# Kernel optimization log

Hardware: AMD Instinct MI355X
Metric: run time of the kernel (lower is better)

The kernel has to match this reference:

```python
import jax, jax.numpy as jnp
import numpy as np


def setup_inputs() -> dict:
    key = jax.random.key(0)
    k1, k2, k3, k4 = jax.random.split(key, 4)
    B, T, S, D = 32, 512, 1024, 1024
    inp = jax.random.normal(k1, (B, T, D), dtype=jnp.float32)
    ctx = jax.random.normal(k2, (B, S, D), dtype=jnp.float32)
    W_in = jax.random.normal(k3, (D, D), dtype=jnp.float32) * (1.0 / np.sqrt(D))
    W_out = jax.random.normal(k4, (D, 2 * D), dtype=jnp.float32) * (1.0 / np.sqrt(2 * D))
    return {"input": inp, "context": ctx, "W_in": W_in, "W_out": W_out}


def reference(input, context, W_in, W_out):
    # GlobalAttention, attn_type='general', no mask, no coverage, tgt_len > 1.
    B, T, D = input.shape
    S = context.shape[1]
    # score: (W_in h_t) . h_s   -> [B, T, S]
    h_t = jnp.einsum('btd,ed->bte', input, W_in)           # linear_in (no bias)
    align = jnp.einsum('btd,bsd->bts', h_t, context)
    align_vectors = jax.nn.softmax(align, axis=-1)          # [B, T, S]
    # weighted sum of context
    c = jnp.einsum('bts,bsd->btd', align_vectors, context)  # [B, T, D]
    # concat [c, input] -> linear_out (no bias for 'general') -> tanh
    concat_c = jnp.concatenate([c, input], axis=-1)          # [B, T, 2D]
    attn_h = jnp.tanh(jnp.einsum('btf,df->btd', concat_c, W_out))
    # not one_step: transpose to [T, B, ...]
    attn_h = jnp.transpose(attn_h, (1, 0, 2))
    align_vectors = jnp.transpose(align_vectors, (1, 0, 2))
    return attn_h, align_vectors
```

## Files before the change

kernel.cpp:

```cpp
#include <hip/hip_runtime.h>
#include <hip/hip_bf16.h>


typedef short bf16x8 __attribute__((ext_vector_type(8)));
typedef float f32x4 __attribute__((ext_vector_type(4)));
typedef unsigned short us;

#define NB 32
#define NT_ 512
#define NS 1024
#define ND 1024

__device__ inline us f2bf(float x) {
  unsigned u = __float_as_uint(x);
  u += 0x7FFFu + ((u >> 16) & 1u);
  return (us)(u >> 16);
}
__device__ inline float bf2f(us h) { return __uint_as_float(((unsigned)h) << 16); }

__device__ inline void store_split(us* __restrict__ hi, us* __restrict__ lo, size_t idx, float v) {
  us h = f2bf(v);
  hi[idx] = h;
  lo[idx] = f2bf(v - bf2f(h));
}

__global__ void ga_split(const float* __restrict__ src, us* __restrict__ hi,
                         us* __restrict__ lo, long n) {
  long i0 = ((long)blockIdx.x * blockDim.x + threadIdx.x) * 4;
  long stride = (long)gridDim.x * blockDim.x * 4;
  for (long i = i0; i < n; i += stride) {
    float4 v = *reinterpret_cast<const float4*>(src + i);
    ushort4 h, l;
    h.x = f2bf(v.x); l.x = f2bf(v.x - bf2f(h.x));
    h.y = f2bf(v.y); l.y = f2bf(v.y - bf2f(h.y));
    h.z = f2bf(v.z); l.z = f2bf(v.z - bf2f(h.z));
    h.w = f2bf(v.w); l.w = f2bf(v.w - bf2f(h.w));
    *reinterpret_cast<ushort4*>(hi + i) = h;
    *reinterpret_cast<ushort4*>(lo + i) = l;
  }
}

__global__ void ga_cvt(const float* __restrict__ src, us* __restrict__ dst, long n) {
  long i0 = ((long)blockIdx.x * blockDim.x + threadIdx.x) * 4;
  long stride = (long)gridDim.x * blockDim.x * 4;
  for (long i = i0; i < n; i += stride) {
    float4 v = *reinterpret_cast<const float4*>(src + i);
    ushort4 h;
    h.x = f2bf(v.x); h.y = f2bf(v.y); h.z = f2bf(v.z); h.w = f2bf(v.w);
    *reinterpret_cast<ushort4*>(dst + i) = h;
  }
}

__global__ void ga_transpose_split(const float* __restrict__ ctx, us* __restrict__ tHi,
                                   us* __restrict__ tLo) {
  __shared__ float tile[64][65];
  int s0 = blockIdx.x << 6, d0 = blockIdx.y << 6, b = blockIdx.z;
  const float* src = ctx + (size_t)b * NS * ND;
  int tid = threadIdx.x;
#pragma unroll
  for (int i = 0; i < 16; ++i) {
    int lin = (i << 8) + tid;
    int r = lin >> 6, c = lin & 63;
    tile[r][c] = src[(size_t)(s0 + r) * ND + d0 + c];
  }
  __syncthreads();
  us* oH = tHi + (size_t)b * ND * NS;
  us* oL = tLo + (size_t)b * ND * NS;
#pragma unroll
  for (int i = 0; i < 16; ++i) {
    int lin = (i << 8) + tid;
    int dr = lin >> 6, sc = lin & 63;
    float v = tile[sc][dr];
    size_t o = (size_t)(d0 + dr) * NS + s0 + sc;
    us h = f2bf(v);
    oH[o] = h;
    oL[o] = f2bf(v - bf2f(h));
  }
}

__global__ __launch_bounds__(256) void ga_softmax(float* __restrict__ al,
                                                  us* __restrict__ pHi, us* __restrict__ pLo) {
  int row = blockIdx.x;
  int tid = threadIdx.x;
  float* p = al + (size_t)row * NS;
  float4 v = *reinterpret_cast<const float4*>(p + (tid << 2));
  float m = fmaxf(fmaxf(v.x, v.y), fmaxf(v.z, v.w));
#pragma unroll
  for (int off = 32; off; off >>= 1) m = fmaxf(m, __shfl_xor(m, off));
  __shared__ float rmax[4], rsum[4];
  int wv = tid >> 6, ln = tid & 63;
  if (ln == 0) rmax[wv] = m;
  __syncthreads();
  m = fmaxf(fmaxf(rmax[0], rmax[1]), fmaxf(rmax[2], rmax[3]));
  float4 e;
  e.x = __expf(v.x - m); e.y = __expf(v.y - m);
  e.z = __expf(v.z - m); e.w = __expf(v.w - m);
  float s = e.x + e.y + e.z + e.w;
#pragma unroll
  for (int off = 32; off; off >>= 1) s += __shfl_xor(s, off);
  if (ln == 0) rsum[wv] = s;
  __syncthreads();
  s = rsum[0] + rsum[1] + rsum[2] + rsum[3];
  float inv = 1.0f / s;
  e.x *= inv; e.y *= inv; e.z *= inv; e.w *= inv;
  *reinterpret_cast<float4*>(p + (tid << 2)) = e;
  int t = row >> 5, b = row & 31;
  size_t o = ((size_t)b * NT_ + t) * NS + (tid << 2);
  ushort4 h, l;
  h.x = f2bf(e.x); l.x = f2bf(e.x - bf2f(h.x));
  h.y = f2bf(e.y); l.y = f2bf(e.y - bf2f(h.y));
  h.z = f2bf(e.z); l.z = f2bf(e.z - bf2f(h.z));
  h.w = f2bf(e.w); l.w = f2bf(e.w - bf2f(h.w));
  *reinterpret_cast<ushort4*>(pHi + o) = h;
  *reinterpret_cast<ushort4*>(pLo + o) = l;
}

__device__ inline void gload16(const us* g, void* l) {
  __builtin_amdgcn_global_load_lds((const __attribute__((address_space(1))) unsigned int*)g,
                                   (__attribute__((address_space(3))) unsigned int*)l, 16, 0, 0);
}

__device__ inline f32x4 mfma16(bf16x8 a, bf16x8 b, f32x4 c) {
  return __builtin_amdgcn_mfma_f32_16x16x32_bf16(a, b, c, 0, 0, 0);
}


#define STG_A(ST, H) do {                                                          \
    int p_ = tid >> 2;                                                             \
    long gr_ = (long)(((p_ >> 6) << 7) + ((H) << 6) + (p_ & 63));                  \
    long sc_ = gr_ * lda + ((tid & 3) << 3) + (long)(ST) * 32;                     \
    char* d_ = lb + (((ST) & 1) ? BUFSZ : 0) + ((H) << 13) + (tid << 4);           \
    const us *ah_, *al_;                                                           \
    if constexpr (MODE == 3) {                                                     \
      if ((ST) < (NT >> 1)) { ah_ = pAh + sc_; al_ = pAl + sc_; }                  \
      else { ah_ = pA2h + sc_ - 1024; al_ = pA2l + sc_ - 1024; }                   \
    } else { ah_ = pAh + sc_; al_ = pAl + sc_; }                                   \
    gload16(ah_, d_);                                                              \
    gload16(al_, d_ + 16384);                                                      \
  } while (0)

#define STG_B(ST) do {                                                             \
    _Pragma("unroll") for (int s_ = 0; s_ < 2; ++s_) {                             \
      int c_ = tid + (s_ << 9);                                                    \
      long sc_ = (long)(c_ >> 2) * ldb + ((c_ & 3) << 3) + (long)(ST) * 32;        \
      char* d_ = lb + (((ST) & 1) ? BUFSZ : 0) + 32768 + (c_ << 4);                \
      gload16(pBh + sc_, d_);                                                      \
      if constexpr (SPLITB) gload16(pBl + sc_, d_ + 16384);                        \
    }                                                                              \
  } while (0)

#define PHASE(H, STAGES, TAIL) do {                                                \
    const char* bp_ = lb + (cur ? BUFSZ : 0);                                      \
    bf16x8 ah_[4], al_[4], bh_[4], bl_[4];                                         \
    _Pragma("unroll") for (int m = 0; m < 4; ++m) {                                \
      ah_[m] = *(const bf16x8*)(bp_ + ((H) << 13) + aoff + (m << 10));             \
      al_[m] = *(const bf16x8*)(bp_ + 16384 + ((H) << 13) + aoff + (m << 10));     \
    }                                                                              \
    _Pragma("unroll") for (int n = 0; n < 4; ++n) {                                \
      bh_[n] = *(const bf16x8*)(bp_ + 32768 + boff + (n << 10));                   \
      if constexpr (SPLITB)                                                        \
        bl_[n] = *(const bf16x8*)(bp_ + 49152 + boff + (n << 10));                 \
    }                                                                              \
    STAGES;                                                                        \
    __builtin_amdgcn_s_barrier();                                                  \
    asm volatile("s_waitcnt lgkmcnt(0)" ::: "memory");                             \
    __builtin_amdgcn_sched_barrier(0);                                             \
    __builtin_amdgcn_s_setprio(1);                                                 \
    _Pragma("unroll") for (int m = 0; m < 4; ++m)                                  \
      _Pragma("unroll") for (int n = 0; n < 4; ++n)                                \
        acc[(H) * 4 + m][n] = mfma16(ah_[m], bh_[n], acc[(H) * 4 + m][n]);         \
    if constexpr (SPLITB)                                                          \
      _Pragma("unroll") for (int m = 0; m < 4; ++m)                                \
        _Pragma("unroll") for (int n = 0; n < 4; ++n)                              \
          acc[(H) * 4 + m][n] = mfma16(ah_[m], bl_[n], acc[(H) * 4 + m][n]);       \
    _Pragma("unroll") for (int m = 0; m < 4; ++m)                                  \
      _Pragma("unroll") for (int n = 0; n < 4; ++n)                                \
        acc[(H) * 4 + m][n] = mfma16(al_[m], bh_[n], acc[(H) * 4 + m][n]);         \
    __builtin_amdgcn_s_setprio(0);                                                 \
    TAIL;                                                                          \
    __builtin_amdgcn_s_barrier();                                                  \
  } while (0)

template <int MODE>
__global__ __launch_bounds__(512, 2) void ga_gmh(
    const us* __restrict__ Ahi, const us* __restrict__ Alo,
    const us* __restrict__ A2hi, const us* __restrict__ A2lo,
    const us* __restrict__ Bhi, const us* __restrict__ Blo,
    void* __restrict__ out0, void* __restrict__ out1,
    int K, int lda, int ldb, long astride, long bstride) {
  constexpr bool SPLITB = (MODE != 3);
  constexpr int BUFSZ = SPLITB ? 65536 : 49152;
  __shared__ __align__(16) char lds[2 * BUFSZ];
  char* lb = lds;
  const int NT = K >> 5;
  const int tid = threadIdx.x;
  const int lane = tid & 63;
  const int wv = tid >> 6;
  const int wr = wv >> 2, wc = wv & 3;
  const int fr = lane & 15;
  const int rowA = blockIdx.x << 8, colB = blockIdx.y << 8;
  const int bz = blockIdx.z;

  const us* pAh = Ahi + (size_t)bz * astride + (size_t)rowA * lda;
  const us* pAl = Alo + (size_t)bz * astride + (size_t)rowA * lda;
  const us* pA2h = (MODE == 3) ? A2hi + (size_t)rowA * lda : nullptr;
  const us* pA2l = (MODE == 3) ? A2lo + (size_t)rowA * lda : nullptr;
  const us* pBh = Bhi + (size_t)bz * bstride + (size_t)colB * ldb;
  const us* pBl = SPLITB ? Blo + (size_t)bz * bstride + (size_t)colB * ldb : nullptr;

  const int aoff = (wr << 12) + (fr << 6) + ((lane >> 4) << 4);
  const int boff = (wc << 12) + (fr << 6) + ((lane >> 4) << 4);

  f32x4 zero = {0.f, 0.f, 0.f, 0.f};
  f32x4 acc[8][4];
#pragma unroll
  for (int i = 0; i < 8; ++i)
#pragma unroll
    for (int k = 0; k < 4; ++k) acc[i][k] = zero;

  STG_A(0, 0); STG_A(0, 1); STG_B(0); STG_A(1, 0);
  asm volatile("s_waitcnt vmcnt(2)" ::: "memory");
  __builtin_amdgcn_s_barrier();

  int cur = 0;
  for (int t = 0; t < NT - 2; ++t) {
    PHASE(0, { STG_B(t + 1); STG_A(t + 1, 1); }, {});
    PHASE(1, { STG_A(t + 2, 0); },
          { asm volatile("s_waitcnt vmcnt(2)" ::: "memory"); });
    cur ^= 1;
  }
  PHASE(0, { STG_B(NT - 1); STG_A(NT - 1, 1); }, {});
  PHASE(1, {}, { asm volatile("s_waitcnt vmcnt(0)" ::: "memory"); });
  cur ^= 1;
  PHASE(0, {}, {});
  PHASE(1, {}, {});

#pragma unroll
  for (int i = 0; i < 8; ++i)
#pragma unroll
    for (int k = 0; k < 4; ++k)
#pragma unroll
      for (int j = 0; j < 4; ++j) {
        int r = rowA + (wr << 7) + ((i >> 2) << 6) + ((i & 3) << 4) + ((lane >> 4) << 2) + j;
        int c = colB + (wc << 6) + (k << 4) + fr;
        float v = acc[i][k][j];
        if constexpr (MODE == 0) {
          store_split((us*)out0, (us*)out1, (size_t)r * 1024 + c, v);
        } else if constexpr (MODE == 1) {
          ((float*)out0)[((size_t)r * NB + bz) * NS + c] = v;
        } else if constexpr (MODE == 2) {
          store_split((us*)out0, (us*)out1, ((size_t)bz * 512 + r) * 1024 + c, v);
        } else {
          int bb = r >> 9, tt2 = r & 511;
          ((float*)out0)[((size_t)tt2 * NB + bb) * ND + c] = tanhf(v);
        }
      }
}

extern "C" void kernel_launch(void* const* d_in, const int* in_sizes, int n_in,
                              void* d_out, int out_size, void* d_ws, size_t ws_size,
                              hipStream_t stream) {
  (void)in_sizes; (void)n_in; (void)out_size; (void)ws_size;
  const float* inp = (const float*)d_in[0];
  const float* ctx = (const float*)d_in[1];
  const float* Win = (const float*)d_in[2];
  const float* Wout = (const float*)d_in[3];
  float* out = (float*)d_out;

  char* w = (char*)d_ws;
  us* ctx_hi  = (us*)(w + 0);
  us* c_hi    = (us*)(w + 0);
  us* c_lo    = (us*)(w + 33554432);
  us* ctx_lo  = (us*)(w + 67108864);
  us* p_hi    = (us*)(w + 67108864);
  us* p_lo    = (us*)(w + 100663296);
  us* in_hi   = (us*)(w + 134217728);
  us* in_lo   = (us*)(w + 167772160);
  us* h_hi    = (us*)(w + 201326592);
  us* h_lo    = (us*)(w + 234881024);
  us* ctxT_lo = (us*)(w + 201326592);
  us* win_hi  = (us*)(w + 268435456);
  us* win_lo  = (us*)(w + 270532608);
  us* wout_b  = (us*)(w + 272629760);

  us* ctxT_hi = (us*)d_out;
  float* alignOut = out + 16777216;

  ga_split<<<2048, 256, 0, stream>>>(inp, in_hi, in_lo, 16777216L);
  ga_split<<<2048, 256, 0, stream>>>(ctx, ctx_hi, ctx_lo, 33554432L);
  ga_split<<<512, 256, 0, stream>>>(Win, win_hi, win_lo, 1048576L);
  ga_cvt<<<512, 256, 0, stream>>>(Wout, wout_b, 2097152L);

  ga_gmh<0><<<dim3(64, 4, 1), 512, 0, stream>>>(in_hi, in_lo, nullptr, nullptr,
                                                win_hi, win_lo, h_hi, h_lo,
                                                1024, 1024, 1024, 0L, 0L);
  ga_gmh<1><<<dim3(2, 4, 32), 512, 0, stream>>>(h_hi, h_lo, nullptr, nullptr,
                                                ctx_hi, ctx_lo, alignOut, nullptr,
                                                1024, 1024, 1024, 524288L, 1048576L);
  ga_transpose_split<<<dim3(16, 16, 32), 256, 0, stream>>>(ctx, ctxT_hi, ctxT_lo);
  ga_softmax<<<16384, 256, 0, stream>>>(alignOut, p_hi, p_lo);
  ga_gmh<2><<<dim3(2, 4, 32), 512, 0, stream>>>(p_hi, p_lo, nullptr, nullptr,
                                                ctxT_hi, ctxT_lo, c_hi, c_lo,
                                                1024, 1024, 1024, 524288L, 1048576L);
  ga_gmh<3><<<dim3(64, 4, 1), 512, 0, stream>>>(c_hi, c_lo, in_hi, in_lo,
                                                wout_b, nullptr, out, nullptr,
                                                2048, 1024, 2048, 0L, 0L);
}
```

Baseline: 677.0 us.

## Switch GEMM kernels to 32x32x16 MFMA with XOR-swizzled LDS layout

Replaces the 16x16x32 bf16 MFMA tiles with 32x32x16 MFMA, reorganising the per-wave accumulator layout, LDS staging addresses and epilogue index mapping. Global-to-LDS loads now write an XOR-swizzled column layout to reduce LDS bank conflicts. The pipeline is simplified to stage a full K-step (A and B) per iteration with a full vmcnt(0) wait, which may expose more memory latency than the previous staggered half-tile prefetch.

```diff
diff --git a/kernel.cpp b/kernel.cpp
--- a/kernel.cpp
+++ b/kernel.cpp
@@ -3,7 +3,7 @@
 
 
 typedef short bf16x8 __attribute__((ext_vector_type(8)));
-typedef float f32x4 __attribute__((ext_vector_type(4)));
+typedef float f32x16 __attribute__((ext_vector_type(16)));
 typedef unsigned short us;
 
 #define NB 32
@@ -120,46 +120,48 @@
                                    (__attribute__((address_space(3))) unsigned int*)l, 16, 0, 0);
 }
 
-__device__ inline f32x4 mfma16(bf16x8 a, bf16x8 b, f32x4 c) {
-  return __builtin_amdgcn_mfma_f32_16x16x32_bf16(a, b, c, 0, 0, 0);
-}
-
-
-#define STG_A(ST, H) do {                                                          \
-    int p_ = tid >> 2;                                                             \
-    long gr_ = (long)(((p_ >> 6) << 7) + ((H) << 6) + (p_ & 63));                  \
-    long sc_ = gr_ * lda + ((tid & 3) << 3) + (long)(ST) * 32;                     \
-    char* d_ = lb + (((ST) & 1) ? BUFSZ : 0) + ((H) << 13) + (tid << 4);           \
+__device__ inline f32x16 mfma32(bf16x8 a, bf16x8 b, f32x16 c) {
+  return __builtin_amdgcn_mfma_f32_32x32x16_bf16(a, b, c, 0, 0, 0);
+}
+
+
+#define STG_A(ST) do {                                                             \
+    long kof_ = (long)(ST) << 5;                                                   \
     const us *ah_, *al_;                                                           \
     if constexpr (MODE == 3) {                                                     \
-      if ((ST) < (NT >> 1)) { ah_ = pAh + sc_; al_ = pAl + sc_; }                  \
-      else { ah_ = pA2h + sc_ - 1024; al_ = pA2l + sc_ - 1024; }                   \
-    } else { ah_ = pAh + sc_; al_ = pAl + sc_; }                                   \
-    gload16(ah_, d_);                                                              \
-    gload16(al_, d_ + 16384);                                                      \
+      if ((ST) < (NT >> 1)) { ah_ = pAh + kof_; al_ = pAl + kof_; }                \
+      else { ah_ = pA2h + kof_ - 1024; al_ = pA2l + kof_ - 1024; }                 \
+    } else { ah_ = pAh + kof_; al_ = pAl + kof_; }                                 \
+    char* d_ = lb + (((ST) & 1) ? BUFSZ : 0) + (tid << 4);                         \
+    gload16(ah_ + gA0, d_);                                                        \
+    gload16(ah_ + gA1, d_ + 8192);                                                 \
+    gload16(al_ + gA0, d_ + 16384);                                                \
+    gload16(al_ + gA1, d_ + 24576);                                                \
   } while (0)
 
 #define STG_B(ST) do {                                                             \
-    _Pragma("unroll") for (int s_ = 0; s_ < 2; ++s_) {                             \
-      int c_ = tid + (s_ << 9);                                                    \
-      long sc_ = (long)(c_ >> 2) * ldb + ((c_ & 3) << 3) + (long)(ST) * 32;        \
-      char* d_ = lb + (((ST) & 1) ? BUFSZ : 0) + 32768 + (c_ << 4);                \
-      gload16(pBh + sc_, d_);                                                      \
-      if constexpr (SPLITB) gload16(pBl + sc_, d_ + 16384);                        \
+    long kof_ = (long)(ST) << 5;                                                   \
+    char* d_ = lb + (((ST) & 1) ? BUFSZ : 0) + 32768 + (tid << 4);                 \
+    gload16(pBh + gB0 + kof_, d_);                                                 \
+    gload16(pBh + gB1 + kof_, d_ + 8192);                                          \
+    if constexpr (SPLITB) {                                                        \
+      gload16(pBl + gB0 + kof_, d_ + 16384);                                       \
+      gload16(pBl + gB1 + kof_, d_ + 24576);                                       \
     }                                                                              \
   } while (0)
 
 #define PHASE(H, STAGES, TAIL) do {                                                \
     const char* bp_ = lb + (cur ? BUFSZ : 0);                                      \
-    bf16x8 ah_[4], al_[4], bh_[4], bl_[4];                                         \
+    const int xb_ = (H) ? xb1 : xb0;                                               \
+    bf16x8 ah_[4], al_[4], bh_[2], bl_[2];                                         \
     _Pragma("unroll") for (int m = 0; m < 4; ++m) {                                \
-      ah_[m] = *(const bf16x8*)(bp_ + ((H) << 13) + aoff + (m << 10));             \
-      al_[m] = *(const bf16x8*)(bp_ + 16384 + ((H) << 13) + aoff + (m << 10));     \
+      ah_[m] = *(const bf16x8*)(bp_ + aBase + (m << 11) + xb_);                    \
+      al_[m] = *(const bf16x8*)(bp_ + 16384 + aBase + (m << 11) + xb_);            \
     }                                                                              \
-    _Pragma("unroll") for (int n = 0; n < 4; ++n) {                                \
-      bh_[n] = *(const bf16x8*)(bp_ + 32768 + boff + (n << 10));                   \
+    _Pragma("unroll") for (int n = 0; n < 2; ++n) {                                \
+      bh_[n] = *(const bf16x8*)(bp_ + 32768 + bBase + (n << 11) + xb_);            \
       if constexpr (SPLITB)                                                        \
-        bl_[n] = *(const bf16x8*)(bp_ + 49152 + boff + (n << 10));                 \
+        bl_[n] = *(const bf16x8*)(bp_ + 49152 + bBase + (n << 11) + xb_);          \
     }                                                                              \
     STAGES;                                                                        \
     __builtin_amdgcn_s_barrier();                                                  \
@@ -167,22 +169,22 @@
     __builtin_amdgcn_sched_barrier(0);                                             \
     __builtin_amdgcn_s_setprio(1);                                                 \
     _Pragma("unroll") for (int m = 0; m < 4; ++m)                                  \
-      _Pragma("unroll") for (int n = 0; n < 4; ++n)                                \
-        acc[(H) * 4 + m][n] = mfma16(ah_[m], bh_[n], acc[(H) * 4 + m][n]);         \
+      _Pragma("unroll") for (int n = 0; n < 2; ++n)                                \
+        acc[m][n] = mfma32(ah_[m], bh_[n], acc[m][n]);                             \
     if constexpr (SPLITB)                                                          \
       _Pragma("unroll") for (int m = 0; m < 4; ++m)                                \
-        _Pragma("unroll") for (int n = 0; n < 4; ++n)                              \
-          acc[(H) * 4 + m][n] = mfma16(ah_[m], bl_[n], acc[(H) * 4 + m][n]);       \
+        _Pragma("unroll") for (int n = 0; n < 2; ++n)                              \
+          acc[m][n] = mfma32(ah_[m], bl_[n], acc[m][n]);                           \
     _Pragma("unroll") for (int m = 0; m < 4; ++m)                                  \
-      _Pragma("unroll") for (int n = 0; n < 4; ++n)                                \
-        acc[(H) * 4 + m][n] = mfma16(al_[m], bh_[n], acc[(H) * 4 + m][n]);         \
+      _Pragma("unroll") for (int n = 0; n < 2; ++n)                                \
+        acc[m][n] = mfma32(al_[m], bh_[n], acc[m][n]);                             \
     __builtin_amdgcn_s_setprio(0);                                                 \
     TAIL;                                                                          \
     __builtin_amdgcn_s_barrier();                                                  \
   } while (0)
 
 template <int MODE>
-__global__ __launch_bounds__(512, 2) void ga_gmh(
+__global__ __launch_bounds__(512, 2) void ga_gm32(
     const us* __restrict__ Ahi, const us* __restrict__ Alo,
     const us* __restrict__ A2hi, const us* __restrict__ A2lo,
     const us* __restrict__ Bhi, const us* __restrict__ Blo,
@@ -195,9 +197,10 @@
   const int NT = K >> 5;
   const int tid = threadIdx.x;
   const int lane = tid & 63;
+  const int l31 = lane & 31;
+  const int hi5 = lane >> 5;
   const int wv = tid >> 6;
   const int wr = wv >> 2, wc = wv & 3;
-  const int fr = lane & 15;
   const int rowA = blockIdx.x << 8, colB = blockIdx.y << 8;
   const int bz = blockIdx.z;
 
@@ -208,42 +211,47 @@
   const us* pBh = Bhi + (size_t)bz * bstride + (size_t)colB * ldb;
   const us* pBl = SPLITB ? Blo + (size_t)bz * bstride + (size_t)colB * ldb : nullptr;
 
-  const int aoff = (wr << 12) + (fr << 6) + ((lane >> 4) << 4);
-  const int boff = (wc << 12) + (fr << 6) + ((lane >> 4) << 4);
-
-  f32x4 zero = {0.f, 0.f, 0.f, 0.f};
-  f32x4 acc[8][4];
-#pragma unroll
-  for (int i = 0; i < 8; ++i)
-#pragma unroll
-    for (int k = 0; k < 4; ++k) acc[i][k] = zero;
-
-  STG_A(0, 0); STG_A(0, 1); STG_B(0); STG_A(1, 0);
-  asm volatile("s_waitcnt vmcnt(2)" ::: "memory");
+  const long swc = (long)(((tid & 3) ^ ((tid >> 3) & 3)) << 3);
+  const long gA0 = (long)(tid >> 2) * lda + swc;
+  const long gA1 = (long)((tid >> 2) + 128) * lda + swc;
+  const long gB0 = (long)(tid >> 2) * ldb + swc;
+  const long gB1 = (long)((tid >> 2) + 128) * ldb + swc;
+
+  const int s_ = (l31 >> 1) & 3;
+  const int xb0 = ((hi5 ^ s_) << 4);
+  const int xb1 = (((2 | hi5) ^ s_) << 4);
+  const int aBase = ((wr << 7) + l31) << 6;
+  const int bBase = ((wc << 6) + l31) << 6;
+
+  f32x16 acc[4][2];
+#pragma unroll
+  for (int m = 0; m < 4; ++m)
+#pragma unroll
+    for (int n = 0; n < 2; ++n)
+#pragma unroll
+      for (int g = 0; g < 16; ++g) acc[m][n][g] = 0.f;
+
+  STG_A(0); STG_B(0);
+  asm volatile("s_waitcnt vmcnt(0)" ::: "memory");
   __builtin_amdgcn_s_barrier();
 
   int cur = 0;
-  for (int t = 0; t < NT - 2; ++t) {
-    PHASE(0, { STG_B(t + 1); STG_A(t + 1, 1); }, {});
-    PHASE(1, { STG_A(t + 2, 0); },
-          { asm volatile("s_waitcnt vmcnt(2)" ::: "memory"); });
+  for (int t = 0; t < NT; ++t) {
+    const bool sg = (t + 1 < NT);
+    PHASE(0, { if (sg) { STG_A(t + 1); STG_B(t + 1); } }, {});
+    PHASE(1, {}, { asm volatile("s_waitcnt vmcnt(0)" ::: "memory"); });
     cur ^= 1;
   }
-  PHASE(0, { STG_B(NT - 1); STG_A(NT - 1, 1); }, {});
-  PHASE(1, {}, { asm volatile("s_waitcnt vmcnt(0)" ::: "memory"); });
-  cur ^= 1;
-  PHASE(0, {}, {});
-  PHASE(1, {}, {});
-
-#pragma unroll
-  for (int i = 0; i < 8; ++i)
-#pragma unroll
-    for (int k = 0; k < 4; ++k)
-#pragma unroll
-      for (int j = 0; j < 4; ++j) {
-        int r = rowA + (wr << 7) + ((i >> 2) << 6) + ((i & 3) << 4) + ((lane >> 4) << 2) + j;
-        int c = colB + (wc << 6) + (k << 4) + fr;
-        float v = acc[i][k][j];
+
+#pragma unroll
+  for (int m = 0; m < 4; ++m)
+#pragma unroll
+    for (int n = 0; n < 2; ++n)
+#pragma unroll
+      for (int g = 0; g < 16; ++g) {
+        int r = rowA + (wr << 7) + (m << 5) + (g & 3) + ((g >> 2) << 3) + (hi5 << 2);
+        int c = colB + (wc << 6) + (n << 5) + l31;
+        float v = acc[m][n][g];
         if constexpr (MODE == 0) {
           store_split((us*)out0, (us*)out1, (size_t)r * 1024 + c, v);
         } else if constexpr (MODE == 1) {
@@ -291,18 +299,18 @@
   ga_split<<<512, 256, 0, stream>>>(Win, win_hi, win_lo, 1048576L);
   ga_cvt<<<512, 256, 0, stream>>>(Wout, wout_b, 2097152L);
 
-  ga_gmh<0><<<dim3(64, 4, 1), 512, 0, stream>>>(in_hi, in_lo, nullptr, nullptr,
-                                                win_hi, win_lo, h_hi, h_lo,
-                                                1024, 1024, 1024, 0L, 0L);
-  ga_gmh<1><<<dim3(2, 4, 32), 512, 0, stream>>>(h_hi, h_lo, nullptr, nullptr,
-                                                ctx_hi, ctx_lo, alignOut, nullptr,
-                                                1024, 1024, 1024, 524288L, 1048576L);
+  ga_gm32<0><<<dim3(64, 4, 1), 512, 0, stream>>>(in_hi, in_lo, nullptr, nullptr,
+                                                 win_hi, win_lo, h_hi, h_lo,
+                                                 1024, 1024, 1024, 0L, 0L);
+  ga_gm32<1><<<dim3(2, 4, 32), 512, 0, stream>>>(h_hi, h_lo, nullptr, nullptr,
+                                                 ctx_hi, ctx_lo, alignOut, nullptr,
+                                                 1024, 1024, 1024, 524288L, 1048576L);
   ga_transpose_split<<<dim3(16, 16, 32), 256, 0, stream>>>(ctx, ctxT_hi, ctxT_lo);
   ga_softmax<<<16384, 256, 0, stream>>>(alignOut, p_hi, p_lo);
-  ga_gmh<2><<<dim3(2, 4, 32), 512, 0, stream>>>(p_hi, p_lo, nullptr, nullptr,
-                                                ctxT_hi, ctxT_lo, c_hi, c_lo,
-                                                1024, 1024, 1024, 524288L, 1048576L);
-  ga_gmh<3><<<dim3(64, 4, 1), 512, 0, stream>>>(c_hi, c_lo, in_hi, in_lo,
-                                                wout_b, nullptr, out, nullptr,
-                                                2048, 1024, 2048, 0L, 0L);
-}
+  ga_gm32<2><<<dim3(2, 4, 32), 512, 0, stream>>>(p_hi, p_lo, nullptr, nullptr,
+                                                 ctxT_hi, ctxT_lo, c_hi, c_lo,
+                                                 1024, 1024, 1024, 524288L, 1048576L);
+  ga_gm32<3><<<dim3(64, 4, 1), 512, 0, stream>>>(c_hi, c_lo, in_hi, in_lo,
+                                                 wout_b, nullptr, out, nullptr,
+                                                 2048, 1024, 2048, 0L, 0L);
+}
```

Result: no change. 682.8 us (+0.8%).

## Restructure split-bf16 GEMM as concatenated-K 256x256x64 tiles with XOR-swizzled LDS

Applied to the files above, without the earlier changes.

Replaces the three-product hi/lo split-bf16 GEMM with a single GEMM over a concatenated K dimension (hi*hi, hi*lo, lo*hi segments, K=3072 or 4096), so each stage streams one A and one B tile. It uses 64-wide K tiles, an XOR swizzle on LDS addresses to reduce bank conflicts, and an eight-phase ping-pong schedule that interleaves global-to-LDS staging with MFMA quadrants. The aim is to cut LDS traffic and bank conflicts and to keep the MFMA units busier. It needs 128KB of LDS per block, which may limit occupancy, and its segment pointer selection is more intricate.

```diff
diff --git a/kernel.cpp b/kernel.cpp
--- a/kernel.cpp
+++ b/kernel.cpp
@@ -125,92 +125,111 @@
 }
 
 
-#define STG_A(ST, H) do {                                                          \
-    int p_ = tid >> 2;                                                             \
-    long gr_ = (long)(((p_ >> 6) << 7) + ((H) << 6) + (p_ & 63));                  \
-    long sc_ = gr_ * lda + ((tid & 3) << 3) + (long)(ST) * 32;                     \
-    char* d_ = lb + (((ST) & 1) ? BUFSZ : 0) + ((H) << 13) + (tid << 4);           \
-    const us *ah_, *al_;                                                           \
-    if constexpr (MODE == 3) {                                                     \
-      if ((ST) < (NT >> 1)) { ah_ = pAh + sc_; al_ = pAl + sc_; }                  \
-      else { ah_ = pA2h + sc_ - 1024; al_ = pA2l + sc_ - 1024; }                   \
-    } else { ah_ = pAh + sc_; al_ = pAl + sc_; }                                   \
-    gload16(ah_, d_);                                                              \
-    gload16(al_, d_ + 16384);                                                      \
-  } while (0)
-
-#define STG_B(ST) do {                                                             \
-    _Pragma("unroll") for (int s_ = 0; s_ < 2; ++s_) {                             \
-      int c_ = tid + (s_ << 9);                                                    \
-      long sc_ = (long)(c_ >> 2) * ldb + ((c_ & 3) << 3) + (long)(ST) * 32;        \
-      char* d_ = lb + (((ST) & 1) ? BUFSZ : 0) + 32768 + (c_ << 4);                \
-      gload16(pBh + sc_, d_);                                                      \
-      if constexpr (SPLITB) gload16(pBl + sc_, d_ + 16384);                        \
+#define VM4 asm volatile("s_waitcnt vmcnt(4)" ::: "memory")
+#define VM0 asm volatile("s_waitcnt vmcnt(0)" ::: "memory")
+
+#define STG_A(T, H) do {                                                           \
+    int s3_ = (T) >> 4;                                                            \
+    const us* ga_ = (MODE == 3)                                                    \
+        ? ((s3_ == 0) ? pA0 : (s3_ == 1) ? pA1 : (s3_ == 2) ? pA2 : pA3)           \
+        : ((s3_ == 2) ? pA1 : pA0);                                                \
+    const us* g_ = ga_ + ((long)((T) & 15) << 6) + ((H) ? aOff1 : aOff0);          \
+    char* d_ = lb + (((T) & 1) << 16) + ((H) << 14) + (tid << 4);                  \
+    gload16(g_, d_);                                                               \
+    gload16(g_ + ald64, d_ + 8192);                                                \
+  } while (0)
+
+#define STG_B(T, H) do {                                                           \
+    int s3_ = (T) >> 4;                                                            \
+    const us* gb_ = (MODE == 3) ? ((s3_ >= 2) ? pB2 : pB0)                         \
+                                : ((s3_ == 1) ? pB1 : pB0);                        \
+    const us* g_ = gb_ + ((long)((T) & 15) << 6) + ((H) ? bOff1 : bOff0);          \
+    char* d_ = lb + (((T) & 1) << 16) + 32768 + ((H) << 14) + (tid << 4);          \
+    gload16(g_, d_);                                                               \
+    gload16(g_ + bld64, d_ + 8192);                                                \
+  } while (0)
+
+#define RD_A(BP, QM) do {                                                          \
+    const char* p_ = (BP) + aRd + ((QM) << 13);                                    \
+    _Pragma("unroll") for (int m_ = 0; m_ < 4; ++m_) {                             \
+      a[m_][0] = *(const bf16x8*)(p_ + (m_ << 11) + colx0);                        \
+      a[m_][1] = *(const bf16x8*)(p_ + (m_ << 11) + colx1);                        \
     }                                                                              \
   } while (0)
 
-#define PHASE(H, STAGES, TAIL) do {                                                \
-    const char* bp_ = lb + (cur ? BUFSZ : 0);                                      \
-    bf16x8 ah_[4], al_[4], bh_[4], bl_[4];                                         \
-    _Pragma("unroll") for (int m = 0; m < 4; ++m) {                                \
-      ah_[m] = *(const bf16x8*)(bp_ + ((H) << 13) + aoff + (m << 10));             \
-      al_[m] = *(const bf16x8*)(bp_ + 16384 + ((H) << 13) + aoff + (m << 10));     \
+#define RD_B(BP, ARR, QN) do {                                                     \
+    const char* p_ = (BP) + bRd + ((QN) << 12);                                    \
+    _Pragma("unroll") for (int n_ = 0; n_ < 2; ++n_) {                             \
+      ARR[n_][0] = *(const bf16x8*)(p_ + (n_ << 11) + colx0);                      \
+      ARR[n_][1] = *(const bf16x8*)(p_ + (n_ << 11) + colx1);                      \
     }                                                                              \
-    _Pragma("unroll") for (int n = 0; n < 4; ++n) {                                \
-      bh_[n] = *(const bf16x8*)(bp_ + 32768 + boff + (n << 10));                   \
-      if constexpr (SPLITB)                                                        \
-        bl_[n] = *(const bf16x8*)(bp_ + 49152 + boff + (n << 10));                 \
-    }                                                                              \
-    STAGES;                                                                        \
+  } while (0)
+
+#define MM(QM, QN, ARR)                                                            \
+  _Pragma("unroll") for (int ks_ = 0; ks_ < 2; ++ks_)                              \
+  _Pragma("unroll") for (int m_ = 0; m_ < 4; ++m_)                                 \
+  _Pragma("unroll") for (int n_ = 0; n_ < 2; ++n_)                                 \
+    acc[(QM) * 4 + m_][(QN) * 2 + n_] =                                            \
+        mfma16(a[m_][ks_], ARR[n_][ks_], acc[(QM) * 4 + m_][(QN) * 2 + n_])
+
+#define PHX(RDS, STGS, TAILV, QM, QN, ARR) do {                                    \
+    RDS;                                                                           \
+    STGS;                                                                          \
     __builtin_amdgcn_s_barrier();                                                  \
     asm volatile("s_waitcnt lgkmcnt(0)" ::: "memory");                             \
     __builtin_amdgcn_sched_barrier(0);                                             \
     __builtin_amdgcn_s_setprio(1);                                                 \
-    _Pragma("unroll") for (int m = 0; m < 4; ++m)                                  \
-      _Pragma("unroll") for (int n = 0; n < 4; ++n)                                \
-        acc[(H) * 4 + m][n] = mfma16(ah_[m], bh_[n], acc[(H) * 4 + m][n]);         \
-    if constexpr (SPLITB)                                                          \
-      _Pragma("unroll") for (int m = 0; m < 4; ++m)                                \
-        _Pragma("unroll") for (int n = 0; n < 4; ++n)                              \
-          acc[(H) * 4 + m][n] = mfma16(ah_[m], bl_[n], acc[(H) * 4 + m][n]);       \
-    _Pragma("unroll") for (int m = 0; m < 4; ++m)                                  \
-      _Pragma("unroll") for (int n = 0; n < 4; ++n)                                \
-        acc[(H) * 4 + m][n] = mfma16(al_[m], bh_[n], acc[(H) * 4 + m][n]);         \
+    MM(QM, QN, ARR);                                                               \
     __builtin_amdgcn_s_setprio(0);                                                 \
-    TAIL;                                                                          \
+    TAILV;                                                                         \
     __builtin_amdgcn_s_barrier();                                                  \
   } while (0)
 
 template <int MODE>
-__global__ __launch_bounds__(512, 2) void ga_gmh(
+__global__ __launch_bounds__(512, 2) void ga_g8(
     const us* __restrict__ Ahi, const us* __restrict__ Alo,
     const us* __restrict__ A2hi, const us* __restrict__ A2lo,
     const us* __restrict__ Bhi, const us* __restrict__ Blo,
     void* __restrict__ out0, void* __restrict__ out1,
     int K, int lda, int ldb, long astride, long bstride) {
-  constexpr bool SPLITB = (MODE != 3);
-  constexpr int BUFSZ = SPLITB ? 65536 : 49152;
-  __shared__ __align__(16) char lds[2 * BUFSZ];
+  __shared__ __align__(16) char lds[131072];
   char* lb = lds;
-  const int NT = K >> 5;
+  const int NTILES = K >> 6;
+  const int NIT = NTILES >> 1;
   const int tid = threadIdx.x;
   const int lane = tid & 63;
+  const int fr = lane & 15;
   const int wv = tid >> 6;
   const int wr = wv >> 2, wc = wv & 3;
-  const int fr = lane & 15;
   const int rowA = blockIdx.x << 8, colB = blockIdx.y << 8;
   const int bz = blockIdx.z;
 
-  const us* pAh = Ahi + (size_t)bz * astride + (size_t)rowA * lda;
-  const us* pAl = Alo + (size_t)bz * astride + (size_t)rowA * lda;
-  const us* pA2h = (MODE == 3) ? A2hi + (size_t)rowA * lda : nullptr;
-  const us* pA2l = (MODE == 3) ? A2lo + (size_t)rowA * lda : nullptr;
-  const us* pBh = Bhi + (size_t)bz * bstride + (size_t)colB * ldb;
-  const us* pBl = SPLITB ? Blo + (size_t)bz * bstride + (size_t)colB * ldb : nullptr;
-
-  const int aoff = (wr << 12) + (fr << 6) + ((lane >> 4) << 4);
-  const int boff = (wc << 12) + (fr << 6) + ((lane >> 4) << 4);
-
+  const us* pA0 = Ahi + (size_t)bz * astride + (size_t)rowA * lda;
+  const us* pA1 = Alo + (size_t)bz * astride + (size_t)rowA * lda;
+  const us* pA2 = (MODE == 3) ? A2hi + (size_t)rowA * lda : nullptr;
+  const us* pA3 = (MODE == 3) ? A2lo + (size_t)rowA * lda : nullptr;
+  const us* pB0 = Bhi + (size_t)bz * bstride + (size_t)colB * ldb;
+  const us* pB1 = (MODE == 3) ? nullptr : Blo + (size_t)bz * bstride + (size_t)colB * ldb;
+  const us* pB2 = (MODE == 3) ? pB0 + 1024 : nullptr;
+
+  const int arow = tid >> 3;
+  const long swe = (long)(((tid & 7) ^ (arow & 7)) << 3);
+  const long aOff0 = (long)arow * lda + swe;
+  const long aOff1 = aOff0 + 128L * lda;
+  const long ald64 = 64L * lda;
+  const long bOff0 = (long)arow * ldb + swe;
+  const long bOff1 = bOff0 + 128L * ldb;
+  const long bld64 = 64L * ldb;
+
+  const int l16 = ((lane >> 4) & 3) << 4;
+  const int colx0 = l16 ^ ((fr & 7) << 4);
+  const int colx1 = colx0 ^ 64;
+  const int aRd = (wr << 14) + (fr << 7);
+  const int bRd = 32768 + ((wc >> 1) << 14) + ((wc & 1) << 13) + (fr << 7);
+  const char* B0P = lb;
+  const char* B1P = lb + 65536;
+
+  bf16x8 a[4][2], b0[2][2], b1[2][2];
   f32x4 zero = {0.f, 0.f, 0.f, 0.f};
   f32x4 acc[8][4];
 #pragma unroll
@@ -218,32 +237,43 @@
 #pragma unroll
     for (int k = 0; k < 4; ++k) acc[i][k] = zero;
 
-  STG_A(0, 0); STG_A(0, 1); STG_B(0); STG_A(1, 0);
-  asm volatile("s_waitcnt vmcnt(2)" ::: "memory");
+  STG_A(0, 0); STG_A(0, 1); STG_B(0, 0); STG_B(0, 1);
+  STG_B(1, 0); STG_B(1, 1);
+  VM4;
   __builtin_amdgcn_s_barrier();
 
-  int cur = 0;
-  for (int t = 0; t < NT - 2; ++t) {
-    PHASE(0, { STG_B(t + 1); STG_A(t + 1, 1); }, {});
-    PHASE(1, { STG_A(t + 2, 0); },
-          { asm volatile("s_waitcnt vmcnt(2)" ::: "memory"); });
-    cur ^= 1;
-  }
-  PHASE(0, { STG_B(NT - 1); STG_A(NT - 1, 1); }, {});
-  PHASE(1, {}, { asm volatile("s_waitcnt vmcnt(0)" ::: "memory"); });
-  cur ^= 1;
-  PHASE(0, {}, {});
-  PHASE(1, {}, {});
-
-#pragma unroll
-  for (int i = 0; i < 8; ++i)
-#pragma unroll
-    for (int k = 0; k < 4; ++k)
+  for (int i = 0; i < NIT - 1; ++i) {
+    const int X = i << 1;
+    PHX({ RD_A(B0P, 0); RD_B(B0P, b0, 0); }, STG_A(X + 1, 0), , 0, 0, b0);
+    PHX(RD_B(B0P, b1, 1),                    STG_A(X + 1, 1), , 0, 1, b1);
+    PHX(RD_A(B0P, 1),                        STG_B(X + 2, 0), , 1, 1, b1);
+    PHX(,                                    STG_B(X + 2, 1), VM4, 1, 0, b0);
+    PHX({ RD_A(B1P, 0); RD_B(B1P, b0, 0); }, STG_A(X + 2, 0), , 0, 0, b0);
+    PHX(RD_B(B1P, b1, 1),                    STG_A(X + 2, 1), , 0, 1, b1);
+    PHX(RD_A(B1P, 1),                        STG_B(X + 3, 0), , 1, 1, b1);
+    PHX(,                                    STG_B(X + 3, 1), VM4, 1, 0, b0);
+  }
+  {
+    const int X = NTILES - 2;
+    PHX({ RD_A(B0P, 0); RD_B(B0P, b0, 0); }, STG_A(X + 1, 0), , 0, 0, b0);
+    PHX(RD_B(B0P, b1, 1),                    STG_A(X + 1, 1), , 0, 1, b1);
+    PHX(RD_A(B0P, 1), , , 1, 1, b1);
+    PHX(, , VM0, 1, 0, b0);
+    PHX({ RD_A(B1P, 0); RD_B(B1P, b0, 0); }, , , 0, 0, b0);
+    PHX(RD_B(B1P, b1, 1), , , 0, 1, b1);
+    PHX(RD_A(B1P, 1), , , 1, 1, b1);
+    PHX(, , , 1, 0, b0);
+  }
+
+#pragma unroll
+  for (int mf = 0; mf < 8; ++mf)
+#pragma unroll
+    for (int nf = 0; nf < 4; ++nf)
 #pragma unroll
       for (int j = 0; j < 4; ++j) {
-        int r = rowA + (wr << 7) + ((i >> 2) << 6) + ((i & 3) << 4) + ((lane >> 4) << 2) + j;
-        int c = colB + (wc << 6) + (k << 4) + fr;
-        float v = acc[i][k][j];
+        int r = rowA + (wr << 7) + (mf << 4) + (((lane >> 4) & 3) << 2) + j;
+        int c = colB + (wc << 6) + (nf << 4) + fr;
+        float v = acc[mf][nf][j];
         if constexpr (MODE == 0) {
           store_split((us*)out0, (us*)out1, (size_t)r * 1024 + c, v);
         } else if constexpr (MODE == 1) {
@@ -291,18 +321,18 @@
   ga_split<<<512, 256, 0, stream>>>(Win, win_hi, win_lo, 1048576L);
   ga_cvt<<<512, 256, 0, stream>>>(Wout, wout_b, 2097152L);
 
-  ga_gmh<0><<<dim3(64, 4, 1), 512, 0, stream>>>(in_hi, in_lo, nullptr, nullptr,
-                                                win_hi, win_lo, h_hi, h_lo,
-                                                1024, 1024, 1024, 0L, 0L);
-  ga_gmh<1><<<dim3(2, 4, 32), 512, 0, stream>>>(h_hi, h_lo, nullptr, nullptr,
-                                                ctx_hi, ctx_lo, alignOut, nullptr,
-                                                1024, 1024, 1024, 524288L, 1048576L);
+  ga_g8<0><<<dim3(64, 4, 1), 512, 0, stream>>>(in_hi, in_lo, nullptr, nullptr,
+                                               win_hi, win_lo, h_hi, h_lo,
+                                               3072, 1024, 1024, 0L, 0L);
+  ga_g8<1><<<dim3(2, 4, 32), 512, 0, stream>>>(h_hi, h_lo, nullptr, nullptr,
+                                               ctx_hi, ctx_lo, alignOut, nullptr,
+                                               3072, 1024, 1024, 524288L, 1048576L);
   ga_transpose_split<<<dim3(16, 16, 32), 256, 0, stream>>>(ctx, ctxT_hi, ctxT_lo);
   ga_softmax<<<16384, 256, 0, stream>>>(alignOut, p_hi, p_lo);
-  ga_gmh<2><<<dim3(2, 4, 32), 512, 0, stream>>>(p_hi, p_lo, nullptr, nullptr,
-                                                ctxT_hi, ctxT_lo, c_hi, c_lo,
-                                                1024, 1024, 1024, 524288L, 1048576L);
-  ga_gmh<3><<<dim3(64, 4, 1), 512, 0, stream>>>(c_hi, c_lo, in_hi, in_lo,
-                                                wout_b, nullptr, out, nullptr,
-                                                2048, 1024, 2048, 0L, 0L);
-}
+  ga_g8<2><<<dim3(2, 4, 32), 512, 0, stream>>>(p_hi, p_lo, nullptr, nullptr,
+                                               ctxT_hi, ctxT_lo, c_hi, c_lo,
+                                               3072, 1024, 1024, 524288L, 1048576L);
+  ga_g8<3><<<dim3(64, 4, 1), 512, 0, stream>>>(c_hi, c_lo, in_hi, in_lo,
+                                               wout_b, nullptr, out, nullptr,
+                                               4096, 1024, 2048, 0L, 0L);
+}
```

After: 619.9 us. 1.09x faster.
